# Performance work log

Hardware: AMD Instinct MI355X
Metric: run time of the kernel (lower is better)

The kernel has to match this reference:

```python
import jax, jax.numpy as jnp
import numpy as np

BATCH, T, C = 32, 600, 64
DEPTH = 2            # logsig depth 2 -> [increments, Levy areas]
N_SEGMENTS = 50
N_HIDDENS = 512
LOGSIG_CH = C + C * (C - 1) // 2   # 2080, Lyndon-word count at depth 2
IN_SIZE = C + LOGSIG_CH            # 2144 = logsig + start point


def _t_vec(nT, n_segments):
    # matches: [int(round(x)) for x in np.linspace(1, nT, n_segments+1)]
    return np.asarray([int(round(v)) for v in np.linspace(1, nT, n_segments + 1)])


def setup_inputs() -> dict:
    key = jax.random.key(0)
    k0, k1, k2, k3, k4 = jax.random.split(key, 5)
    x = jax.random.normal(k0, (BATCH, T, C), jnp.float32)
    s = 1.0 / np.sqrt(N_HIDDENS)
    w_ih = jax.random.uniform(k1, (4 * N_HIDDENS, IN_SIZE), jnp.float32, -s, s)
    w_hh = jax.random.uniform(k2, (4 * N_HIDDENS, N_HIDDENS), jnp.float32, -s, s)
    b_ih = jax.random.uniform(k3, (4 * N_HIDDENS,), jnp.float32, -s, s)
    b_hh = jax.random.uniform(k4, (4 * N_HIDDENS,), jnp.float32, -s, s)
    return {"x": x, "w_ih": w_ih, "w_hh": w_hh, "b_ih": b_ih, "b_hh": b_hh}


def _logsig_and_start(x):
    """Depth-2 segmented log-signature + segment start points.
    Returns (logsig (B,S,LOGSIG_CH), start (B,S,C))."""
    B, nT, c = x.shape
    tv = _t_vec(nT, N_SEGMENTS)
    starts = tv[:-1] - 1               # segment start frame indices
    ends = tv[1:] - 1                  # segment end frame indices
    # step s (between frames s and s+1) belongs to segment i iff tv[i]-1 <= s < tv[i+1]-1
    step_ids = jnp.asarray(np.searchsorted(tv[1:] - 1, np.arange(nT - 1), side='right'))
    dx = x[:, 1:] - x[:, :-1]                            # (B, T-1, C)
    # per-step outer product x_{t-} (X) dx_t, then segmented sum over steps
    prod = jnp.einsum('btc,btd->btcd', x[:, :-1], dx)    # (B, T-1, C, C)
    Q = jax.ops.segment_sum(jnp.moveaxis(prod, 1, 0), step_ids,
                            num_segments=N_SEGMENTS)      # (S, B, C, C)
    xa = x[:, starts]                                    # (B, S, C)
    xb = x[:, ends]
    inc = xb - xa                                        # level-1 logsig
    # shift origin to segment start: P = sum (X_rel (X) dX)
    P = jnp.moveaxis(Q, 0, 1) - jnp.einsum('bsc,bsd->bscd', xa, inc)
    A = 0.5 * (P - jnp.swapaxes(P, -1, -2))              # Levy area (antisym)
    iu, ju = np.triu_indices(c, 1)                       # Lyndon words (i,j), i<j, lex order
    logsig = jnp.concatenate([inc, A[:, :, iu, ju]], axis=-1)
    return logsig, xa


def _lstm(feats, w_ih, w_hh, b_ih, b_hh):
    B = feats.shape[0]
    H = N_HIDDENS
    gx = jnp.einsum('bsf,gf->bsg', feats, w_ih) + b_ih + b_hh  # (B,S,4H)

    def step(carry, g_t):
        h, cc = carry
        g = g_t + h @ w_hh.T
        i, f, gg, o = jnp.split(g, 4, axis=-1)
        i = jax.nn.sigmoid(i); f = jax.nn.sigmoid(f)
        gg = jnp.tanh(gg); o = jax.nn.sigmoid(o)
        cc = f * cc + i * gg
        h = o * jnp.tanh(cc)
        return (h, cc), h

    h0 = jnp.zeros((B, H), feats.dtype)
    (_, _), hs = jax.lax.scan(step, (h0, h0), jnp.moveaxis(gx, 1, 0))
    return jnp.moveaxis(hs, 0, 1)                        # (B, S, H)


def reference(x, w_ih, w_hh, b_ih, b_hh):
    logsig, x_sp = _logsig_and_start(x)
    feats = jnp.concatenate([logsig, x_sp], axis=-1)      # (B, S, IN_SIZE)
    return _lstm(feats, w_ih, w_hh, b_ih, b_hh)
```

## Files before the change

### kernel.cpp

```cpp
#include <hip/hip_runtime.h>
#include <math.h>

typedef _Float16 f16;
typedef _Float16 f16x8 __attribute__((ext_vector_type(8)));
typedef _Float16 f16x4 __attribute__((ext_vector_type(4)));
typedef float    f32x4 __attribute__((ext_vector_type(4)));

#define BATCH 32
#define TT    600
#define CC    64
#define SEG   50
#define HH    512
#define G4    2048
#define FF    2144
#define MM    1600
#define MP    1664
#define NPAIR 2016
#define CVB   512
#define WRK   208
#define SLOT16 16384
#define KT    67
#define BUFB  12288

struct TV { int v[51]; };

__device__ __forceinline__ void async_copy16(char* lds, const char* g) {
  __builtin_amdgcn_global_load_lds(
      (const __attribute__((address_space(1))) unsigned int*)g,
      (__attribute__((address_space(3))) unsigned int*)lds, 16, 0, 0);
}

__device__ __forceinline__ float sigm(float x) { return 1.f / (1.f + __expf(-x)); }
__device__ __forceinline__ float tanh_(float x) {
  float ax = fabsf(x);
  float e  = __expf(2.f * ax);
  float t  = 1.f - 2.f / (e + 1.f);
  return x < 0.f ? -t : t;
}
__device__ __forceinline__ unsigned short f16_bits(f16 v) {
  union { f16 f; unsigned short u; } c; c.f = v; return c.u;
}
__device__ __forceinline__ unsigned int f32_bits(float v) {
  union { float f; unsigned int u; } c; c.f = v; return c.u;
}

__global__ void prep_kernel(const float* __restrict__ x, f16* __restrict__ fhi, TV tv,
                            const float4* __restrict__ w_ih, const float4* __restrict__ w_hh,
                            f16x4* __restrict__ w16, f16x4* __restrict__ whh16,
                            unsigned int* __restrict__ ready) {
  __shared__ float xs[13 * CC];
  int m   = blockIdx.x;
  int tid = threadIdx.x;

  if (m >= MP) {
    int cb   = m - MP;
    int gtid = cb * 256 + tid;
    int nth  = CVB * 256;
    for (int i = gtid; i < G4 * FF / 4; i += nth) {
      float4 v = w_ih[i];
      f16x4 o = {(f16)v.x, (f16)v.y, (f16)v.z, (f16)v.w};
      w16[i] = o;
    }
    for (int i = gtid; i < G4 * HH / 4; i += nth) {
      float4 v = w_hh[i];
      f16x4 o = {(f16)v.x, (f16)v.y, (f16)v.z, (f16)v.w};
      whh16[i] = o;
    }
    if (cb == 0)
      for (int i = tid; i < 544; i += 256) ready[i] = 0u;
    return;
  }

  f16* rhi = fhi + (size_t)m * FF;
  if (m >= MM) {
    unsigned int* a = (unsigned int*)rhi;
    for (int i = tid; i < FF / 2; i += 256) a[i] = 0u;
    return;
  }
  int bb = m & 31, ss = m >> 5;
  int t0 = tv.v[ss] - 1, t1 = tv.v[ss + 1] - 1;
  int len = t1 - t0;
  for (int i = tid; i < (len + 1) * CC; i += 256)
    xs[i] = x[(size_t)bb * TT * CC + (size_t)(t0 + (i >> 6)) * CC + (i & 63)];
  __syncthreads();

  if (tid < CC) {
    float xa  = xs[tid];
    float inc = xs[len * CC + tid] - xa;
    rhi[tid] = (f16)inc;
    rhi[2080 + tid] = (f16)xa;
  }

  int p0 = tid * 8;
  if (p0 < NPAIR) {
    int c = 0, rem = p0;
    while (rem >= 63 - c) { rem -= 63 - c; c++; }
    int d = c + 1 + rem;
    int cs[8], dd[8];
#pragma unroll
    for (int i = 0; i < 8; i++) {
      cs[i] = c; dd[i] = d;
      d++; if (d == 64) { c++; d = c + 1; }
    }
    float acc[8], xc[8], xd[8];
#pragma unroll
    for (int i = 0; i < 8; i++) { acc[i] = 0.f; xc[i] = xs[cs[i]]; xd[i] = xs[dd[i]]; }
    for (int t = 1; t <= len; t++) {
#pragma unroll
      for (int i = 0; i < 8; i++) {
        float nc = xs[t * CC + cs[i]], nd = xs[t * CC + dd[i]];
        acc[i] += xc[i] * (nd - xd[i]) - xd[i] * (nc - xc[i]);
        xc[i] = nc; xd[i] = nd;
      }
    }
#pragma unroll
    for (int i = 0; i < 8; i++) {
      int ci = cs[i], di = dd[i];
      float xac = xs[ci], xad = xs[di];
      float incc = xs[len * CC + ci] - xac, incd = xs[len * CC + di] - xad;
      float v = 0.5f * acc[i] - 0.5f * (xac * incd - xad * incc);
      rhi[64 + p0 + i] = (f16)v;
    }
  }
}

__global__ __launch_bounds__(256) void fused_kernel(
    const f16* __restrict__ fhi, const f16* __restrict__ w16,
    const float* __restrict__ bih, const float* __restrict__ bhh,
    const f16* __restrict__ whh16, float* __restrict__ gx,
    unsigned short* __restrict__ hbuf, unsigned int* __restrict__ ready,
    unsigned int* __restrict__ gxcnt, float* __restrict__ out) {
  __shared__ __align__(16) char smem[61440];
  int tid  = threadIdx.x;
  int lane = tid & 63;

  if (blockIdx.x >= 32) {
    int w  = blockIdx.x - 32;
    int wn = tid >> 6;
    int rowq = tid >> 2;
    int ldst = tid * 16;
    int quad = lane >> 4;
    int am   = lane & 15;
    unsigned int* gxa = (unsigned int*)gx;

    int qsrc = ((tid & 3) ^ ((tid >> 3) & 3)) * 8;

    int offA[4], offB[2];
#pragma unroll
    for (int mi = 0; mi < 4; mi++) {
      int ra = mi * 16 + am;
      offA[mi] = ra * 64 + ((quad ^ ((ra >> 1) & 3)) * 16);
    }
#pragma unroll
    for (int ni = 0; ni < 2; ni++) {
      int rb = wn * 32 + ni * 16 + am;
      offB[ni] = 4096 + rb * 64 + ((quad ^ ((rb >> 1) & 3)) * 16);
    }

    for (int t = 0; t < 2; t++) {
      int id = w + t * WRK;
      int mt = id >> 4, nt = id & 15;
      int m0 = mt * 64, n0 = nt * 128;

      const f16* pa  = fhi + (size_t)(m0 + rowq) * FF + qsrc;
      const f16* pb0 = w16 + (size_t)(n0 + rowq) * FF + qsrc;
      const f16* pb1 = pb0 + (size_t)64 * FF;

      f32x4 zero4 = {0.f, 0.f, 0.f, 0.f};
      f32x4 acc[4][2];
#pragma unroll
      for (int i = 0; i < 4; i++) { acc[i][0] = zero4; acc[i][1] = zero4; }

      for (int kp = 0; kp < 3; kp++) {
        char* b = smem + kp * BUFB;
        int koff = kp * 32;
        async_copy16(b + ldst,        (const char*)(pa + koff));
        async_copy16(b + 4096 + ldst, (const char*)(pb0 + koff));
        async_copy16(b + 8192 + ldst, (const char*)(pb1 + koff));
      }

      for (int kt = 0; kt < KT; kt++) {
        if (kt + 3 < KT) {
          char* b = smem + ((kt + 3) % 5) * BUFB;
          int koff = (kt + 3) * 32;
          async_copy16(b + ldst,        (const char*)(pa + koff));
          async_copy16(b + 4096 + ldst, (const char*)(pb0 + koff));
          async_copy16(b + 8192 + ldst, (const char*)(pb1 + koff));
          asm volatile("s_waitcnt vmcnt(9)" ::: "memory");
        } else if (kt + 3 == KT) {
          asm volatile("s_waitcnt vmcnt(6)" ::: "memory");
        } else if (kt + 2 == KT) {
          asm volatile("s_waitcnt vmcnt(3)" ::: "memory");
        } else {
          asm volatile("s_waitcnt vmcnt(0)" ::: "memory");
        }
        __builtin_amdgcn_s_barrier();
        __builtin_amdgcn_sched_barrier(0);

        char* bb = smem + (kt % 5) * BUFB;
        f16x8 bfr[2];
        bfr[0] = *(const f16x8*)(bb + offB[0]);
        bfr[1] = *(const f16x8*)(bb + offB[1]);
#pragma unroll
        for (int mi = 0; mi < 4; mi++) {
          f16x8 ah = *(const f16x8*)(bb + offA[mi]);
#pragma unroll
          for (int ni = 0; ni < 2; ni++)
            acc[mi][ni] = __builtin_amdgcn_mfma_f32_16x16x32_f16(ah, bfr[ni], acc[mi][ni], 0, 0, 0);
        }
      }

#pragma unroll
      for (int ni = 0; ni < 2; ni++) {
        int ncol = n0 + wn * 32 + ni * 16 + (lane & 15);
        float bv = bih[ncol] + bhh[ncol];
#pragma unroll
        for (int mi = 0; mi < 4; mi++) {
          int mrow = m0 + mi * 16 + (lane >> 4) * 4;
#pragma unroll
          for (int r = 0; r < 4; r++)
            __hip_atomic_store(gxa + (size_t)(mrow + r) * G4 + ncol,
                               f32_bits(acc[mi][ni][r] + bv),
                               __ATOMIC_RELAXED, __HIP_MEMORY_SCOPE_AGENT);
        }
      }
      __syncthreads();
      if (tid == 0)
        __hip_atomic_fetch_add(&gxcnt[mt], 1u, __ATOMIC_RELAXED,
                               __HIP_MEMORY_SCOPE_AGENT);
    }
    return;
  }

  f16* hs = (f16*)smem;
  float* gb = (float*)(smem + 32768);

  int gate = tid >> 6;
  int u0   = blockIdx.x * 16;
  int wg   = blockIdx.x;

  f16x8 bf[16];
  {
    const f16* wrow = whh16 + (size_t)(gate * HH + u0 + (lane & 15)) * HH + (lane >> 4) * 8;
#pragma unroll
    for (int ks = 0; ks < 16; ks++) bf[ks] = *(const f16x8*)(wrow + ks * 32);
  }

  int b1 = tid >> 4;
  int ul = tid & 15;
  float cst0 = 0.f, cst1 = 0.f;
  int aq  = (lane >> 4);
  int am  = (lane & 15);
  int col = lane & 15;
  int rbase = (lane >> 4) * 4;

  for (int s = 0; s < SEG; s++) {
    {
      unsigned tgt = (unsigned)s;
      int mt = s >> 1;
      bool needg = ((s & 1) == 0);
      for (;;) {
        bool ok = true;
        if (s > 0)
          ok = __hip_atomic_load(&ready[(lane & 31) * 16], __ATOMIC_RELAXED,
                                 __HIP_MEMORY_SCOPE_AGENT) >= tgt;
        if (needg)
          ok = ok && (__hip_atomic_load(&gxcnt[mt], __ATOMIC_RELAXED,
                                        __HIP_MEMORY_SCOPE_AGENT) >= 16u);
        if (__all(ok)) break;
        __builtin_amdgcn_s_sleep(1);
      }
      asm volatile("" ::: "memory");
    }

    if (s > 0) {
      const char* hrd = (const char*)(hbuf + (size_t)s * SLOT16);
#pragma unroll
      for (int c = 0; c < 8; c++)
        async_copy16((char*)hs + c * 4096 + tid * 16, hrd + c * 4096 + tid * 16);
    }

    float gxr0[4], gxr1[4];
#pragma unroll
    for (int r = 0; r < 4; r++) {
      int b = rbase + r;
      gxr0[r] = gx[(size_t)((s << 5) + b) * G4 + gate * HH + u0 + col];
      gxr1[r] = gx[(size_t)((s << 5) + b + 16) * G4 + gate * HH + u0 + col];
    }

    f32x4 acc0 = {0.f, 0.f, 0.f, 0.f};
    f32x4 acc1 = {0.f, 0.f, 0.f, 0.f};

    if (s > 0) {
      __syncthreads();

#pragma unroll
      for (int ks = 0; ks < 16; ks++) {
        f16x8 a0 = *(const f16x8*)((char*)hs + (((ks * 4 + aq) * 32) + am) * 16);
        f16x8 a1 = *(const f16x8*)((char*)hs + (((ks * 4 + aq) * 32) + 16 + am) * 16);
        acc0 = __builtin_amdgcn_mfma_f32_16x16x32_f16(a0, bf[ks], acc0, 0, 0, 0);
        acc1 = __builtin_amdgcn_mfma_f32_16x16x32_f16(a1, bf[ks], acc1, 0, 0, 0);
      }
    }

#pragma unroll
    for (int r = 0; r < 4; r++) {
      int b = rbase + r;
      gb[(gate * 32 + b) * 16 + col]      = acc0[r] + gxr0[r];
      gb[(gate * 32 + b + 16) * 16 + col] = acc1[r] + gxr1[r];
    }
    __syncthreads();

    unsigned short* hwr = hbuf + (size_t)(s + 1) * SLOT16;
    int k = u0 + ul;
    float h0, h1;
    {
      float i_ = sigm(gb[(0 * 32 + b1) * 16 + ul]), f_ = sigm(gb[(1 * 32 + b1) * 16 + ul]);
      float g_ = tanh_(gb[(2 * 32 + b1) * 16 + ul]), o_ = sigm(gb[(3 * 32 + b1) * 16 + ul]);
      cst0 = f_ * cst0 + i_ * g_;
      h0 = o_ * tanh_(cst0);
    }
    {
      int b2 = b1 + 16;
      float i_ = sigm(gb[(0 * 32 + b2) * 16 + ul]), f_ = sigm(gb[(1 * 32 + b2) * 16 + ul]);
      float g_ = tanh_(gb[(2 * 32 + b2) * 16 + ul]), o_ = sigm(gb[(3 * 32 + b2) * 16 + ul]);
      cst1 = f_ * cst1 + i_ * g_;
      h1 = o_ * tanh_(cst1);
    }

    if (s < SEG - 1) {
      __hip_atomic_store(hwr + ((k >> 3) * 32 + b1) * 8 + (k & 7),
                         f16_bits((f16)h0), __ATOMIC_RELAXED, __HIP_MEMORY_SCOPE_AGENT);
      __hip_atomic_store(hwr + ((k >> 3) * 32 + (b1 + 16)) * 8 + (k & 7),
                         f16_bits((f16)h1), __ATOMIC_RELAXED, __HIP_MEMORY_SCOPE_AGENT);
      __syncthreads();
      if (tid == 0)
        __hip_atomic_store(&ready[wg * 16], (unsigned int)(s + 1),
                           __ATOMIC_RELAXED, __HIP_MEMORY_SCOPE_AGENT);
    }

    out[(size_t)(b1 * SEG + s) * HH + k] = h0;
    out[(size_t)((b1 + 16) * SEG + s) * HH + k] = h1;
  }
}

extern "C" void kernel_launch(void* const* d_in, const int* in_sizes, int n_in,
                              void* d_out, int out_size, void* d_ws, size_t ws_size,
                              hipStream_t stream) {
  const float* x    = (const float*)d_in[0];
  const float* w_ih = (const float*)d_in[1];
  const float* w_hh = (const float*)d_in[2];
  const float* b_ih = (const float*)d_in[3];
  const float* b_hh = (const float*)d_in[4];
  float* out = (float*)d_out;

  char* ws = (char*)d_ws;
  f16*   fhi   = (f16*)(ws + 0);
  f16*   w16   = (f16*)(ws + 7135232);
  f16*   whh16 = (f16*)(ws + 15921152);
  float* gx    = (float*)(ws + 18018304);
  unsigned short* hbuf  = (unsigned short*)(ws + 31649792);
  unsigned int*   ready = (unsigned int*)(ws + 33288192);

  TV tv;
  double step = 599.0 / 50.0;
  for (int i = 0; i <= 50; i++) {
    double v = (double)i * step + 1.0;
    tv.v[i] = (int)nearbyint(v);
  }
  tv.v[50] = 600;

  unsigned int* gxcnt = ready + 512;

  prep_kernel<<<dim3(MP + CVB), dim3(256), 0, stream>>>(
      x, fhi, tv, (const float4*)w_ih, (const float4*)w_hh,
      (f16x4*)w16, (f16x4*)whh16, ready);

  fused_kernel<<<dim3(32 + WRK), dim3(256), 0, stream>>>(
      fhi, w16, b_ih, b_hh, whh16, gx, hbuf, ready, gxcnt, out);
}
```

Baseline: 262.3 us.

## Poll readiness from one wave and split h-tile load into two pipelined halves

Measured after the change: 249.8 us. -4.8%, faster.

```diff
diff --git a/kernel.cpp b/kernel.cpp
--- a/kernel.cpp
+++ b/kernel.cpp
@@ -255,51 +255,71 @@
   int rbase = (lane >> 4) * 4;
 
   for (int s = 0; s < SEG; s++) {
-    {
+    if (tid < 64) {
+      bool needh = (s > 0) && (lane < 32);
+      bool needg = ((s & 1) == 0) && (lane == 32);
       unsigned tgt = (unsigned)s;
-      int mt = s >> 1;
-      bool needg = ((s & 1) == 0);
+      int mtx = s >> 1;
       for (;;) {
         bool ok = true;
-        if (s > 0)
-          ok = __hip_atomic_load(&ready[(lane & 31) * 16], __ATOMIC_RELAXED,
+        if (needh)
+          ok = __hip_atomic_load(&ready[lane * 16], __ATOMIC_RELAXED,
                                  __HIP_MEMORY_SCOPE_AGENT) >= tgt;
         if (needg)
-          ok = ok && (__hip_atomic_load(&gxcnt[mt], __ATOMIC_RELAXED,
+          ok = ok && (__hip_atomic_load(&gxcnt[mtx], __ATOMIC_RELAXED,
                                         __HIP_MEMORY_SCOPE_AGENT) >= 16u);
         if (__all(ok)) break;
         __builtin_amdgcn_s_sleep(1);
       }
-      asm volatile("" ::: "memory");
-    }
+    }
+    __builtin_amdgcn_s_barrier();
+    asm volatile("" ::: "memory");
+    __builtin_amdgcn_sched_barrier(0);
+
+    f32x4 acc0 = {0.f, 0.f, 0.f, 0.f};
+    f32x4 acc1 = {0.f, 0.f, 0.f, 0.f};
+    float gxr0[4], gxr1[4];
 
     if (s > 0) {
       const char* hrd = (const char*)(hbuf + (size_t)s * SLOT16);
 #pragma unroll
       for (int c = 0; c < 8; c++)
         async_copy16((char*)hs + c * 4096 + tid * 16, hrd + c * 4096 + tid * 16);
-    }
-
-    float gxr0[4], gxr1[4];
-#pragma unroll
-    for (int r = 0; r < 4; r++) {
-      int b = rbase + r;
-      gxr0[r] = gx[(size_t)((s << 5) + b) * G4 + gate * HH + u0 + col];
-      gxr1[r] = gx[(size_t)((s << 5) + b + 16) * G4 + gate * HH + u0 + col];
-    }
-
-    f32x4 acc0 = {0.f, 0.f, 0.f, 0.f};
-    f32x4 acc1 = {0.f, 0.f, 0.f, 0.f};
-
-    if (s > 0) {
-      __syncthreads();
-
-#pragma unroll
-      for (int ks = 0; ks < 16; ks++) {
+
+      asm volatile("s_waitcnt vmcnt(4)" ::: "memory");
+      __builtin_amdgcn_s_barrier();
+      __builtin_amdgcn_sched_barrier(0);
+
+#pragma unroll
+      for (int r = 0; r < 4; r++) {
+        int b = rbase + r;
+        gxr0[r] = gx[(size_t)((s << 5) + b) * G4 + gate * HH + u0 + col];
+        gxr1[r] = gx[(size_t)((s << 5) + b + 16) * G4 + gate * HH + u0 + col];
+      }
+#pragma unroll
+      for (int ks = 0; ks < 8; ks++) {
         f16x8 a0 = *(const f16x8*)((char*)hs + (((ks * 4 + aq) * 32) + am) * 16);
         f16x8 a1 = *(const f16x8*)((char*)hs + (((ks * 4 + aq) * 32) + 16 + am) * 16);
         acc0 = __builtin_amdgcn_mfma_f32_16x16x32_f16(a0, bf[ks], acc0, 0, 0, 0);
         acc1 = __builtin_amdgcn_mfma_f32_16x16x32_f16(a1, bf[ks], acc1, 0, 0, 0);
+      }
+
+      asm volatile("s_waitcnt vmcnt(8)" ::: "memory");
+      __builtin_amdgcn_s_barrier();
+      __builtin_amdgcn_sched_barrier(0);
+#pragma unroll
+      for (int ks = 8; ks < 16; ks++) {
+        f16x8 a0 = *(const f16x8*)((char*)hs + (((ks * 4 + aq) * 32) + am) * 16);
+        f16x8 a1 = *(const f16x8*)((char*)hs + (((ks * 4 + aq) * 32) + 16 + am) * 16);
+        acc0 = __builtin_amdgcn_mfma_f32_16x16x32_f16(a0, bf[ks], acc0, 0, 0, 0);
+        acc1 = __builtin_amdgcn_mfma_f32_16x16x32_f16(a1, bf[ks], acc1, 0, 0, 0);
+      }
+    } else {
+#pragma unroll
+      for (int r = 0; r < 4; r++) {
+        int b = rbase + r;
+        gxr0[r] = gx[(size_t)((s << 5) + b) * G4 + gate * HH + u0 + col];
+        gxr1[r] = gx[(size_t)((s << 5) + b + 16) * G4 + gate * HH + u0 + col];
       }
     }
 
@@ -337,6 +357,8 @@
       if (tid == 0)
         __hip_atomic_store(&ready[wg * 16], (unsigned int)(s + 1),
                            __ATOMIC_RELAXED, __HIP_MEMORY_SCOPE_AGENT);
+    } else {
+      __syncthreads();
     }
 
     out[(size_t)(b1 * SEG + s) * HH + k] = h0;
```

## Split input-projection GEMM along K with atomic accumulation and restructure recurrence waits

Applied to the files above, without the earlier changes.

Result: faster. 240.7 us (-8.2%).

```diff
diff --git a/kernel.cpp b/kernel.cpp
--- a/kernel.cpp
+++ b/kernel.cpp
@@ -19,7 +19,6 @@
 #define CVB   512
 #define WRK   208
 #define SLOT16 16384
-#define KT    67
 #define BUFB  12288
 
 struct TV { int v[51]; };
@@ -40,14 +39,13 @@
 __device__ __forceinline__ unsigned short f16_bits(f16 v) {
   union { f16 f; unsigned short u; } c; c.f = v; return c.u;
 }
-__device__ __forceinline__ unsigned int f32_bits(float v) {
-  union { float f; unsigned int u; } c; c.f = v; return c.u;
-}
 
 __global__ void prep_kernel(const float* __restrict__ x, f16* __restrict__ fhi, TV tv,
                             const float4* __restrict__ w_ih, const float4* __restrict__ w_hh,
                             f16x4* __restrict__ w16, f16x4* __restrict__ whh16,
-                            unsigned int* __restrict__ ready) {
+                            unsigned int* __restrict__ ready,
+                            const float* __restrict__ bih, const float* __restrict__ bhh,
+                            float4* __restrict__ gx4) {
   __shared__ float xs[13 * CC];
   int m   = blockIdx.x;
   int tid = threadIdx.x;
@@ -65,6 +63,13 @@
       float4 v = w_hh[i];
       f16x4 o = {(f16)v.x, (f16)v.y, (f16)v.z, (f16)v.w};
       whh16[i] = o;
+    }
+    for (int i = gtid; i < MP * (G4 / 4); i += nth) {
+      int c4 = i & (G4 / 4 - 1);
+      float4 bi = ((const float4*)bih)[c4];
+      float4 bh = ((const float4*)bhh)[c4];
+      float4 o = {bi.x + bh.x, bi.y + bh.y, bi.z + bh.z, bi.w + bh.w};
+      gx4[i] = o;
     }
     if (cb == 0)
       for (int i = tid; i < 544; i += 256) ready[i] = 0u;
@@ -141,7 +146,6 @@
     int ldst = tid * 16;
     int quad = lane >> 4;
     int am   = lane & 15;
-    unsigned int* gxa = (unsigned int*)gx;
 
     int qsrc = ((tid & 3) ^ ((tid >> 3) & 3)) * 8;
 
@@ -157,13 +161,18 @@
       offB[ni] = 4096 + rb * 64 + ((quad ^ ((rb >> 1) & 3)) * 16);
     }
 
-    for (int t = 0; t < 2; t++) {
-      int id = w + t * WRK;
-      int mt = id >> 4, nt = id & 15;
+    for (int t = 0; t < 4; t++) {
+      int id  = w + t * WRK;
+      int nt  = id & 15;
+      int mtk = id >> 4;
+      int kh  = mtk & 1;
+      int mt  = mtk >> 1;
       int m0 = mt * 64, n0 = nt * 128;
-
-      const f16* pa  = fhi + (size_t)(m0 + rowq) * FF + qsrc;
-      const f16* pb0 = w16 + (size_t)(n0 + rowq) * FF + qsrc;
+      int kbase = kh * 1088;
+      int KTh  = kh ? 33 : 34;
+
+      const f16* pa  = fhi + (size_t)(m0 + rowq) * FF + kbase + qsrc;
+      const f16* pb0 = w16 + (size_t)(n0 + rowq) * FF + kbase + qsrc;
       const f16* pb1 = pb0 + (size_t)64 * FF;
 
       f32x4 zero4 = {0.f, 0.f, 0.f, 0.f};
@@ -179,17 +188,17 @@
         async_copy16(b + 8192 + ldst, (const char*)(pb1 + koff));
       }
 
-      for (int kt = 0; kt < KT; kt++) {
-        if (kt + 3 < KT) {
+      for (int kt = 0; kt < KTh; kt++) {
+        if (kt + 3 < KTh) {
           char* b = smem + ((kt + 3) % 5) * BUFB;
           int koff = (kt + 3) * 32;
           async_copy16(b + ldst,        (const char*)(pa + koff));
           async_copy16(b + 4096 + ldst, (const char*)(pb0 + koff));
           async_copy16(b + 8192 + ldst, (const char*)(pb1 + koff));
           asm volatile("s_waitcnt vmcnt(9)" ::: "memory");
-        } else if (kt + 3 == KT) {
+        } else if (kt + 3 == KTh) {
           asm volatile("s_waitcnt vmcnt(6)" ::: "memory");
-        } else if (kt + 2 == KT) {
+        } else if (kt + 2 == KTh) {
           asm volatile("s_waitcnt vmcnt(3)" ::: "memory");
         } else {
           asm volatile("s_waitcnt vmcnt(0)" ::: "memory");
@@ -212,16 +221,15 @@
 
 #pragma unroll
       for (int ni = 0; ni < 2; ni++) {
-        int ncol = n0 + wn * 32 + ni * 16 + (lane & 15);
-        float bv = bih[ncol] + bhh[ncol];
+        int ncol = n0 + wn * 32 + ni * 16 + am;
 #pragma unroll
         for (int mi = 0; mi < 4; mi++) {
-          int mrow = m0 + mi * 16 + (lane >> 4) * 4;
+          int mrow = m0 + mi * 16 + quad * 4;
 #pragma unroll
           for (int r = 0; r < 4; r++)
-            __hip_atomic_store(gxa + (size_t)(mrow + r) * G4 + ncol,
-                               f32_bits(acc[mi][ni][r] + bv),
-                               __ATOMIC_RELAXED, __HIP_MEMORY_SCOPE_AGENT);
+            __hip_atomic_fetch_add(&gx[(size_t)(mrow + r) * G4 + ncol],
+                                   acc[mi][ni][r],
+                                   __ATOMIC_RELAXED, __HIP_MEMORY_SCOPE_AGENT);
         }
       }
       __syncthreads();
@@ -255,29 +263,13 @@
   int rbase = (lane >> 4) * 4;
 
   for (int s = 0; s < SEG; s++) {
-    {
-      unsigned tgt = (unsigned)s;
-      int mt = s >> 1;
-      bool needg = ((s & 1) == 0);
-      for (;;) {
-        bool ok = true;
-        if (s > 0)
-          ok = __hip_atomic_load(&ready[(lane & 31) * 16], __ATOMIC_RELAXED,
-                                 __HIP_MEMORY_SCOPE_AGENT) >= tgt;
-        if (needg)
-          ok = ok && (__hip_atomic_load(&gxcnt[mt], __ATOMIC_RELAXED,
-                                        __HIP_MEMORY_SCOPE_AGENT) >= 16u);
-        if (__all(ok)) break;
-        __builtin_amdgcn_s_sleep(1);
-      }
-      asm volatile("" ::: "memory");
-    }
-
-    if (s > 0) {
-      const char* hrd = (const char*)(hbuf + (size_t)s * SLOT16);
-#pragma unroll
-      for (int c = 0; c < 8; c++)
-        async_copy16((char*)hs + c * 4096 + tid * 16, hrd + c * 4096 + tid * 16);
+    if ((s & 1) == 0) {
+      if (tid == 0) {
+        while (__hip_atomic_load(&gxcnt[s >> 1], __ATOMIC_RELAXED,
+                                 __HIP_MEMORY_SCOPE_AGENT) < 32u)
+          __builtin_amdgcn_s_sleep(1);
+      }
+      __syncthreads();
     }
 
     float gxr0[4], gxr1[4];
@@ -292,6 +284,18 @@
     f32x4 acc1 = {0.f, 0.f, 0.f, 0.f};
 
     if (s > 0) {
+      unsigned int tgt = (unsigned int)s;
+      if (tid < 32) {
+        while (__hip_atomic_load(&ready[tid * 16], __ATOMIC_RELAXED,
+                                 __HIP_MEMORY_SCOPE_AGENT) < tgt)
+          __builtin_amdgcn_s_sleep(1);
+      }
+      __syncthreads();
+
+      const char* hrd = (const char*)(hbuf + (size_t)s * SLOT16);
+#pragma unroll
+      for (int c = 0; c < 8; c++)
+        async_copy16((char*)hs + c * 4096 + tid * 16, hrd + c * 4096 + tid * 16);
       __syncthreads();
 
 #pragma unroll
@@ -374,7 +378,7 @@
 
   prep_kernel<<<dim3(MP + CVB), dim3(256), 0, stream>>>(
       x, fhi, tv, (const float4*)w_ih, (const float4*)w_hh,
-      (f16x4*)w16, (f16x4*)whh16, ready);
+      (f16x4*)w16, (f16x4*)whh16, ready, b_ih, b_hh, (float4*)gx);
 
   fused_kernel<<<dim3(32 + WRK), dim3(256), 0, stream>>>(
       fhi, w16, b_ih, b_hh, whh16, gx, hbuf, ready, gxcnt, out);
```
